# Optimization experiments

Measured on AMD Instinct MI355X. Metric: run time of the kernel, lower is better.

Reference implementation:

```python
import jax, jax.numpy as jnp
import numpy as np

SPAN = 128
STRIDE = 4
LQ = 2048
LKV = 512
H = 16
DQK = 64
DV = 64
DQ = 1024
DOUT = 1024
T = SPAN // STRIDE  # table depth (rows of the sparse QK table)


def _tables():
    # Static precomputation mirroring the torch __init__ meshgrid logic.
    row, col = np.meshgrid(np.arange(T), np.arange(LQ), indexing='ij')
    qi_col = np.ceil((col - (SPAN - 1)) / STRIDE).astype(np.int64) + row  # kv index per (r, j)
    qi_row = -STRIDE * qi_col + col
    valid = (qi_row >= 0) & (qi_row < SPAN) & (qi_col >= 0) & (qi_col < LKV)
    kidx = np.clip(qi_col, 0, LKV - 1)  # clipped gather index; invalid slots masked later
    return jnp.asarray(kidx), jnp.asarray(valid)

KIDX, VALID = _tables()  # both [T, LQ]


def setup_inputs() -> dict:
    key = jax.random.key(0)
    ks = jax.random.split(key, 7)
    s = 0.02
    return {
        'q': jax.random.normal(ks[0], (2, LQ, DQ), jnp.float32),
        'k': jax.random.normal(ks[1], (2, LKV, DQ), jnp.float32),
        'v': jax.random.normal(ks[2], (2, LKV, DQ), jnp.float32),
        'Wq': jax.random.normal(ks[3], (DQ, H * DQK), jnp.float32) * s,
        'Wk': jax.random.normal(ks[4], (DQ, H * DQK), jnp.float32) * s,
        'Wv': jax.random.normal(ks[5], (DQ, H * DV), jnp.float32) * s,
        'Wo': jax.random.normal(ks[6], (H * DV, DOUT), jnp.float32) * s,
    }


def reference(q, k, v, Wq, Wk, Wv, Wo):
    B = q.shape[0]
    Q = (q @ Wq).reshape(B, LQ, H, DQK).transpose(0, 2, 1, 3)    # [B,H,LQ,DQK]
    K = (k @ Wk).reshape(B, LKV, H, DQK).transpose(0, 2, 1, 3)   # [B,H,LKV,DQK]
    V = (v @ Wv).reshape(B, LKV, H, DV).transpose(0, 2, 1, 3)    # [B,H,LKV,DV]

    # Gather K/V by the strided-span index table: [B,H,T,LQ,d]
    Kg = K[:, :, KIDX, :]
    Vg = V[:, :, KIDX, :]

    scores = jnp.einsum('bhjd,bhtjd->bhtj', Q, Kg) / np.float32(np.sqrt(DQK))
    scores = jnp.where(VALID, scores, -jnp.inf)
    probs = jax.nn.softmax(scores, axis=2)          # softmax over table rows (dim 2 in torch)
    probs = jnp.where(VALID, probs, 0.0)

    O = jnp.einsum('bhtj,bhtjd->bhjd', probs, Vg)   # [B,H,LQ,DV]
    O = O.transpose(0, 2, 1, 3).reshape(B, LQ, H * DV)
    return O @ Wo
```

## Files before the change

### kernel.cpp

```cpp
#include <hip/hip_runtime.h>
#include <hip/hip_bf16.h>

typedef __bf16 bf16x8 __attribute__((ext_vector_type(8)));
typedef float  f32x4  __attribute__((ext_vector_type(4)));
typedef unsigned short u16;
typedef unsigned int   u32;

__device__ __forceinline__ u16 f2b(float x) {
  __bf16 b = (__bf16)x;
  return __builtin_bit_cast(u16, b);
}

__device__ __forceinline__ void gload_lds16(const u16* g, u16* l) {
  __builtin_amdgcn_global_load_lds(
      (const __attribute__((address_space(1))) void*)g,
      (__attribute__((address_space(3))) void*)l, 16, 0, 0);
}

__device__ __forceinline__ void cvt8_store(u16* dst, float4 a, float4 b) {
  union { u16 u[8]; uint4 v; } r;
  r.u[0] = f2b(a.x); r.u[1] = f2b(a.y); r.u[2] = f2b(a.z); r.u[3] = f2b(a.w);
  r.u[4] = f2b(b.x); r.u[5] = f2b(b.y); r.u[6] = f2b(b.z); r.u[7] = f2b(b.w);
  *(uint4*)dst = r.v;
}

__global__ __launch_bounds__(256) void prep_kernel(
    const float* __restrict__ W0, const float* __restrict__ W1,
    const float* __restrict__ W2, const float* __restrict__ W3,
    u16* __restrict__ T0, u16* __restrict__ T1, u16* __restrict__ T2, u16* __restrict__ T3)
{
  __shared__ float tile[32][33];
  int t = blockIdx.x;
  int z = t >> 10, rem = t & 1023;
  const float* W = (z == 0) ? W0 : (z == 1) ? W1 : (z == 2) ? W2 : W3;
  u16* T = (z == 0) ? T0 : (z == 1) ? T1 : (z == 2) ? T2 : T3;
  int tx = threadIdx.x & 31, ty = threadIdx.x >> 5;
  int c0 = (rem & 31) << 5, r0 = (rem >> 5) << 5;
#pragma unroll
  for (int i = 0; i < 4; ++i)
    tile[ty + i * 8][tx] = W[(size_t)(r0 + ty + i * 8) * 1024 + c0 + tx];
  __syncthreads();
#pragma unroll
  for (int i = 0; i < 4; ++i)
    T[(size_t)(c0 + ty + i * 8) * 1024 + r0 + tx] = f2b(tile[tx][ty + i * 8]);
}

__device__ __forceinline__ void compute_step(
    const u16* asc, const u16* bsc, int lane, int wm, int wn, f32x4 (&acc)[4][4])
{
#pragma unroll
  for (int kk = 0; kk < 2; ++kk) {
    bf16x8 af[4], bfr[4];
    int colb = (kk << 6) + ((lane >> 4) << 4);
#pragma unroll
    for (int m = 0; m < 4; ++m) {
      int r = (wm << 6) + (m << 4) + (lane & 15);
      af[m] = *(const bf16x8*)((const char*)asc + (r << 7) + (colb ^ ((r & 7) << 4)));
    }
#pragma unroll
    for (int n = 0; n < 4; ++n) {
      int r = (wn << 6) + (n << 4) + (lane & 15);
      bfr[n] = *(const bf16x8*)((const char*)bsc + (r << 7) + (colb ^ ((r & 7) << 4)));
    }
#pragma unroll
    for (int m = 0; m < 4; ++m)
#pragma unroll
      for (int n = 0; n < 4; ++n)
        acc[m][n] = __builtin_amdgcn_mfma_f32_16x16x32_bf16(af[m], bfr[n], acc[m][n], 0, 0, 0);
  }
}

__device__ __forceinline__ void stage_b(const u16* gB, u16* bs, int wave, int K, int k0) {
#pragma unroll
  for (int i = 0; i < 4; ++i) {
    int rb = (wave << 5) + (i << 3);
    gload_lds16(gB + (size_t)(i << 3) * K + k0, bs + (rb << 6));
  }
}

template <int OUTF32>
__device__ __forceinline__ void cwrite(
    void* C, int N, int row0, int col0, int lane, int wm, int wn, f32x4 (&acc)[4][4])
{
  const int crow = (lane >> 4) << 2;
  const int ccol = lane & 15;
#pragma unroll
  for (int m = 0; m < 4; ++m) {
#pragma unroll
    for (int n = 0; n < 4; ++n) {
      int r = row0 + (wm << 6) + (m << 4) + crow;
      int c = col0 + (wn << 6) + (n << 4) + ccol;
#pragma unroll
      for (int reg = 0; reg < 4; ++reg) {
        if (OUTF32) ((float*)C)[(size_t)(r + reg) * N + c] = acc[m][n][reg];
        else        ((u16*)C)[(size_t)(r + reg) * N + c] = f2b(acc[m][n][reg]);
      }
    }
  }
}

template <int OUTF32>
__device__ __forceinline__ void gemm_core(
    const u16* __restrict__ A, const u16* __restrict__ Bt, void* __restrict__ C,
    int N, int K, int row0, int col0,
    u16* As0, u16* As1, u16* Bs0, u16* Bs1)
{
  const int tid = threadIdx.x;
  const int wave = tid >> 6, lane = tid & 63;
  const int wm = wave >> 1, wn = wave & 1;
  f32x4 acc[4][4] = {};

  const int srow = lane >> 3, sslot = lane & 7;
  const int scol = ((sslot ^ srow) << 3);
  const u16* gA = A + (size_t)(row0 + (wave << 5) + srow) * K + scol;
  const u16* gB = Bt + (size_t)(col0 + (wave << 5) + srow) * K + scol;

  stage_b(gA, As0, wave, K, 0);
  stage_b(gB, Bs0, wave, K, 0);
  __syncthreads();

  u16 *asc = As0, *bsc = Bs0, *asn = As1, *bsn = Bs1;
  for (int k0 = 0; k0 < K; k0 += 64) {
    if (k0 + 64 < K) {
      stage_b(gA, asn, wave, K, k0 + 64);
      stage_b(gB, bsn, wave, K, k0 + 64);
    }
    compute_step(asc, bsc, lane, wm, wn, acc);
    __syncthreads();
    u16* t_;
    t_ = asc; asc = asn; asn = t_;
    t_ = bsc; bsc = bsn; bsn = t_;
  }
  cwrite<OUTF32>(C, N, row0, col0, lane, wm, wn, acc);
}

__device__ __forceinline__ void gemm_core_f32a(
    const float* __restrict__ Af,
    const u16* __restrict__ Bt, u16* __restrict__ C,
    int N, int K, int row0, int col0,
    u16* As0, u16* As1, u16* Bs0, u16* Bs1)
{
  const int tid = threadIdx.x;
  const int wave = tid >> 6, lane = tid & 63;
  const int wm = wave >> 1, wn = wave & 1;
  f32x4 acc[4][4] = {};

  const int srow = lane >> 3, sslot = lane & 7;
  const int scol = ((sslot ^ srow) << 3);
  const float* gAf = Af + (size_t)((wave << 5) + srow) * K + scol;
  const u16*  gB  = Bt + (size_t)(col0 + (wave << 5) + srow) * K + scol;
  const int awbase = (lane << 3);

  float4 a0[4], a1[4];
#pragma unroll
  for (int i = 0; i < 4; ++i) {
    const float* g = gAf + (size_t)(i << 3) * K;
    a0[i] = *(const float4*)g; a1[i] = *(const float4*)(g + 4);
  }
  stage_b(gB, Bs0, wave, K, 0);
#pragma unroll
  for (int i = 0; i < 4; ++i)
    cvt8_store(As0 + (((wave << 5) + (i << 3)) << 6) + awbase, a0[i], a1[i]);
  __syncthreads();

  u16 *asc = As0, *bsc = Bs0, *asn = As1, *bsn = Bs1;
  for (int k0 = 0; k0 < K; k0 += 64) {
    const bool more = (k0 + 64) < K;
    if (more) {
#pragma unroll
      for (int i = 0; i < 4; ++i) {
        const float* g = gAf + (size_t)(i << 3) * K + (k0 + 64);
        a0[i] = *(const float4*)g; a1[i] = *(const float4*)(g + 4);
      }
      stage_b(gB, bsn, wave, K, k0 + 64);
    }
    compute_step(asc, bsc, lane, wm, wn, acc);
    __syncthreads();
    if (more) {
#pragma unroll
      for (int i = 0; i < 4; ++i)
        cvt8_store(asn + (((wave << 5) + (i << 3)) << 6) + awbase, a0[i], a1[i]);
    }
    __syncthreads();
    u16* t_;
    t_ = asc; asc = asn; asn = t_;
    t_ = bsc; bsc = bsn; bsn = t_;
  }
  cwrite<0>(C, N, row0, col0, lane, wm, wn, acc);
}

template <int OUTF32>
__global__ __launch_bounds__(256, 2) void gemm_bt_kernel(
    const u16* __restrict__ A, const u16* __restrict__ Bt, void* __restrict__ C,
    int M, int N, int K)
{
  __shared__ u16 As[2][8192];
  __shared__ u16 Bs[2][8192];
  int bid = blockIdx.x;
  int t = (bid & 7) * 32 + (bid >> 3);
  const int bx = t & 7, by = t >> 3;
  gemm_core<OUTF32>(A, Bt, C, N, K, by << 7, bx << 7, As[0], As[1], Bs[0], Bs[1]);
}

__global__ __launch_bounds__(256, 2) void proj_kernel(
    const float* __restrict__ q, const float* __restrict__ k, const float* __restrict__ v,
    const u16* __restrict__ Wqt, const u16* __restrict__ Wkt, const u16* __restrict__ Wvt,
    u16* __restrict__ Qp, u16* __restrict__ KVp)
{
  __shared__ u16 As[2][8192];
  __shared__ u16 Bs[2][8192];
  int bid = blockIdx.x;
  int t = (bid & 7) * 48 + (bid >> 3);
  const float* Af; const u16* Bt; u16* C; int row0, col0;
  if (t < 256) {
    row0 = (t >> 3) << 7; col0 = (t & 7) << 7;
    Af = q + (size_t)row0 * 1024; Bt = Wqt; C = Qp;
  } else {
    int t2 = t - 256;
    row0 = (t2 >> 3) << 7; col0 = (t2 & 7) << 7;
    if (row0 < 1024) { Af = k + (size_t)row0 * 1024; Bt = Wkt; }
    else             { Af = v + (size_t)(row0 - 1024) * 1024; Bt = Wvt; }
    C = KVp;
  }
  gemm_core_f32a(Af, Bt, C, 1024, 1024, row0, col0, As[0], As[1], Bs[0], Bs[1]);
}

#define VTP 56
#define PLP 72
__global__ __launch_bounds__(256) void attn_kernel(
    const u16* __restrict__ Qp, const u16* __restrict__ Kp,
    const u16* __restrict__ Vp, u16* __restrict__ Ob)
{
  __shared__ u16 Ql[64 * 64];
  __shared__ u16 Kl[48 * 64];
  __shared__ u16 Vt[64 * VTP + 64];
  __shared__ u16 Pl[64 * PLP];

  const int jt = blockIdx.x, h = blockIdx.y, b = blockIdx.z;
  const int j0 = jt << 6;
  const int kbase = (j0 - 124) >> 2;
  const int tid = threadIdx.x;
  const int wave = tid >> 6, lane = tid & 63;

  const int srow = lane >> 3, sslot = lane & 7;
  const int scol = ((sslot ^ srow) << 3);
  for (int g = wave; g < 8; g += 4) {
    int r = (g << 3) + srow;
    const u16* ga = Qp + (((size_t)(b * 2048 + j0 + r)) << 10) + (h << 6) + scol;
    gload_lds16(ga, &Ql[g << 9]);
  }
  for (int g = wave; g < 6; g += 4) {
    int r = (g << 3) + srow;
    int key = kbase + r;
    key = key < 0 ? 0 : (key > 511 ? 511 : key);
    const u16* gk = Kp + (((size_t)(b * 512 + key)) << 10) + (h << 6) + scol;
    gload_lds16(gk, &Kl[g << 9]);
  }
  for (int idx = tid; idx < 48 * 8; idx += 256) {
    int row = idx >> 3, seg = idx & 7;
    int key = kbase + row;
    key = key < 0 ? 0 : (key > 511 ? 511 : key);
    uint4 x = *(const uint4*)(Vp + (((size_t)(b * 512 + key)) << 10) + (h << 6) + (seg << 3));
    int d0 = seg << 3;
    Vt[(d0 + 0) * VTP + row] = (u16)(x.x);
    Vt[(d0 + 1) * VTP + row] = (u16)(x.x >> 16);
    Vt[(d0 + 2) * VTP + row] = (u16)(x.y);
    Vt[(d0 + 3) * VTP + row] = (u16)(x.y >> 16);
    Vt[(d0 + 4) * VTP + row] = (u16)(x.z);
    Vt[(d0 + 5) * VTP + row] = (u16)(x.z >> 16);
    Vt[(d0 + 6) * VTP + row] = (u16)(x.w);
    Vt[(d0 + 7) * VTP + row] = (u16)(x.w >> 16);
  }
  if (tid < 64) *(uint4*)&Vt[tid * VTP + 48] = make_uint4(0, 0, 0, 0);
  else if (tid < 72) *(uint4*)&Vt[64 * VTP + ((tid - 64) << 3)] = make_uint4(0, 0, 0, 0);
  __syncthreads();

  f32x4 sacc[3] = {};
  const int frow_a = (wave << 4) + (lane & 15);
#pragma unroll
  for (int kk = 0; kk < 2; ++kk) {
    int colb = (kk << 6) + ((lane >> 4) << 4);
    bf16x8 aq = *(const bf16x8*)((const char*)Ql + (frow_a << 7) + (colb ^ ((frow_a & 7) << 4)));
#pragma unroll
    for (int nt = 0; nt < 3; ++nt) {
      int rk = (nt << 4) + (lane & 15);
      bf16x8 bk = *(const bf16x8*)((const char*)Kl + (rk << 7) + (colb ^ ((rk & 7) << 4)));
      sacc[nt] = __builtin_amdgcn_mfma_f32_16x16x32_bf16(aq, bk, sacc[nt], 0, 0, 0);
    }
  }

  const int rof = (wave << 2) + (lane >> 4);
  const int cb0 = lane & 15;
  bool vld[3]; float sc[3][4];
#pragma unroll
  for (int nt = 0; nt < 3; ++nt) {
    int c = cb0 + (nt << 4);
    vld[nt] = ((unsigned)(c - rof) < 32u) && (kbase + c >= 0);
#pragma unroll
    for (int r = 0; r < 4; ++r) sc[nt][r] = sacc[nt][r] * 0.125f;
  }
  float mx[4], rs[4];
#pragma unroll
  for (int r = 0; r < 4; ++r) {
    float m = -3.0e38f;
#pragma unroll
    for (int nt = 0; nt < 3; ++nt) m = vld[nt] ? fmaxf(m, sc[nt][r]) : m;
    m = fmaxf(m, __shfl_xor(m, 1));
    m = fmaxf(m, __shfl_xor(m, 2));
    m = fmaxf(m, __shfl_xor(m, 4));
    m = fmaxf(m, __shfl_xor(m, 8));
    mx[r] = m;
  }
#pragma unroll
  for (int r = 0; r < 4; ++r) {
    float s = 0.f;
#pragma unroll
    for (int nt = 0; nt < 3; ++nt) {
      float e = vld[nt] ? __expf(sc[nt][r] - mx[r]) : 0.f;
      sc[nt][r] = e;
      s += e;
    }
    s += __shfl_xor(s, 1);
    s += __shfl_xor(s, 2);
    s += __shfl_xor(s, 4);
    s += __shfl_xor(s, 8);
    rs[r] = 1.f / s;
  }
#pragma unroll
  for (int r = 0; r < 4; ++r) {
    int jq = (wave << 4) + ((lane >> 4) << 2) + r;
#pragma unroll
    for (int nt = 0; nt < 3; ++nt)
      Pl[jq * PLP + cb0 + (nt << 4)] = f2b(sc[nt][r] * rs[r]);
    Pl[jq * PLP + 48 + cb0] = 0;
  }
  __syncthreads();

  f32x4 oacc[4] = {};
#pragma unroll
  for (int kk = 0; kk < 2; ++kk) {
    int koff = (kk << 5) + ((lane >> 4) << 3);
    bf16x8 ap = *(const bf16x8*)&Pl[frow_a * PLP + koff];
#pragma unroll
    for (int nt = 0; nt < 4; ++nt) {
      int dr = (nt << 4) + (lane & 15);
      bf16x8 bv = *(const bf16x8*)&Vt[dr * VTP + koff];
      oacc[nt] = __builtin_amdgcn_mfma_f32_16x16x32_bf16(ap, bv, oacc[nt], 0, 0, 0);
    }
  }

#pragma unroll
  for (int nt = 0; nt < 4; ++nt) {
    int d = (nt << 4) + (lane & 15);
#pragma unroll
    for (int r = 0; r < 4; ++r) {
      int jq = (wave << 4) + ((lane >> 4) << 2) + r;
      Ob[(((size_t)(b * 2048 + j0 + jq)) << 10) + (h << 6) + d] = f2b(oacc[nt][r]);
    }
  }
}

extern "C" void kernel_launch(void* const* d_in, const int* in_sizes, int n_in,
                              void* d_out, int out_size, void* d_ws, size_t ws_size,
                              hipStream_t stream) {
  const float* q  = (const float*)d_in[0];
  const float* k  = (const float*)d_in[1];
  const float* v  = (const float*)d_in[2];
  const float* Wq = (const float*)d_in[3];
  const float* Wk = (const float*)d_in[4];
  const float* Wv = (const float*)d_in[5];
  const float* Wo = (const float*)d_in[6];

  char* ws = (char*)d_ws;
  const size_t MB = 1u << 20;
  u16* Wqt = (u16*)(ws + 0 * MB);
  u16* Wkt = (u16*)(ws + 2 * MB);
  u16* Wvt = (u16*)(ws + 4 * MB);
  u16* Wot = (u16*)(ws + 6 * MB);
  u16* Qp  = (u16*)(ws + 8 * MB);
  u16* Kp  = (u16*)(ws + 16 * MB);
  u16* Vp  = (u16*)(ws + 18 * MB);
  u16* Ob  = (u16*)(ws + 20 * MB);

  prep_kernel<<<4096, 256, 0, stream>>>(Wq, Wk, Wv, Wo, Wqt, Wkt, Wvt, Wot);
  proj_kernel<<<384, 256, 0, stream>>>(q, k, v, Wqt, Wkt, Wvt, Qp, Kp);
  attn_kernel<<<dim3(32, 16, 2), 256, 0, stream>>>(Qp, Kp, Vp, Ob);
  gemm_bt_kernel<1><<<256, 256, 0, stream>>>(Ob, Wot, d_out, 4096, 1024, 1024);
}
```

Before: 59.63 us.

## Move Wo transpose into attention kernel and remap attention block order

```diff
diff --git a/kernel.cpp b/kernel.cpp
--- a/kernel.cpp
+++ b/kernel.cpp
@@ -24,25 +24,31 @@
   *(uint4*)dst = r.v;
 }
 
+__device__ __forceinline__ void wtile_transpose(
+    const float* __restrict__ W, u16* __restrict__ T, int rem, float* tile )
+{
+  int tx = threadIdx.x & 31, ty = threadIdx.x >> 5;
+  int c0 = (rem & 31) << 5, r0 = (rem >> 5) << 5;
+#pragma unroll
+  for (int i = 0; i < 4; ++i)
+    tile[(ty + i * 8) * 33 + tx] = W[(size_t)(r0 + ty + i * 8) * 1024 + c0 + tx];
+  __syncthreads();
+#pragma unroll
+  for (int i = 0; i < 4; ++i)
+    T[(size_t)(c0 + ty + i * 8) * 1024 + r0 + tx] = f2b(tile[tx * 33 + ty + i * 8]);
+}
+
 __global__ __launch_bounds__(256) void prep_kernel(
     const float* __restrict__ W0, const float* __restrict__ W1,
-    const float* __restrict__ W2, const float* __restrict__ W3,
-    u16* __restrict__ T0, u16* __restrict__ T1, u16* __restrict__ T2, u16* __restrict__ T3)
-{
-  __shared__ float tile[32][33];
+    const float* __restrict__ W2,
+    u16* __restrict__ T0, u16* __restrict__ T1, u16* __restrict__ T2)
+{
+  __shared__ float tile[32 * 33];
   int t = blockIdx.x;
   int z = t >> 10, rem = t & 1023;
-  const float* W = (z == 0) ? W0 : (z == 1) ? W1 : (z == 2) ? W2 : W3;
-  u16* T = (z == 0) ? T0 : (z == 1) ? T1 : (z == 2) ? T2 : T3;
-  int tx = threadIdx.x & 31, ty = threadIdx.x >> 5;
-  int c0 = (rem & 31) << 5, r0 = (rem >> 5) << 5;
-#pragma unroll
-  for (int i = 0; i < 4; ++i)
-    tile[ty + i * 8][tx] = W[(size_t)(r0 + ty + i * 8) * 1024 + c0 + tx];
-  __syncthreads();
-#pragma unroll
-  for (int i = 0; i < 4; ++i)
-    T[(size_t)(c0 + ty + i * 8) * 1024 + r0 + tx] = f2b(tile[tx][ty + i * 8]);
+  const float* W = (z == 0) ? W0 : (z == 1) ? W1 : W2;
+  u16* T = (z == 0) ? T0 : (z == 1) ? T1 : T2;
+  wtile_transpose(W, T, rem, tile);
 }
 
 __device__ __forceinline__ void compute_step(
@@ -229,14 +235,21 @@
 #define PLP 72
 __global__ __launch_bounds__(256) void attn_kernel(
     const u16* __restrict__ Qp, const u16* __restrict__ Kp,
-    const u16* __restrict__ Vp, u16* __restrict__ Ob)
+    const u16* __restrict__ Vp, u16* __restrict__ Ob,
+    const float* __restrict__ W3, u16* __restrict__ T3)
 {
   __shared__ u16 Ql[64 * 64];
   __shared__ u16 Kl[48 * 64];
   __shared__ u16 Vt[64 * VTP + 64];
   __shared__ u16 Pl[64 * PLP];
 
-  const int jt = blockIdx.x, h = blockIdx.y, b = blockIdx.z;
+  const int bid = blockIdx.x;
+  if (bid >= 1024) {
+    wtile_transpose(W3, T3, bid - 1024, (float*)Ql);
+    return;
+  }
+  const int t = (bid & 7) * 128 + (bid >> 3);
+  const int jt = t & 31, h = (t >> 5) & 15, b = t >> 9;
   const int j0 = jt << 6;
   const int kbase = (j0 - 124) >> 2;
   const int tid = threadIdx.x;
@@ -382,8 +395,8 @@
   u16* Vp  = (u16*)(ws + 18 * MB);
   u16* Ob  = (u16*)(ws + 20 * MB);
 
-  prep_kernel<<<4096, 256, 0, stream>>>(Wq, Wk, Wv, Wo, Wqt, Wkt, Wvt, Wot);
+  prep_kernel<<<3072, 256, 0, stream>>>(Wq, Wk, Wv, Wqt, Wkt, Wvt);
   proj_kernel<<<384, 256, 0, stream>>>(q, k, v, Wqt, Wkt, Wvt, Qp, Kp);
-  attn_kernel<<<dim3(32, 16, 2), 256, 0, stream>>>(Qp, Kp, Vp, Ob);
+  attn_kernel<<<2048, 256, 0, stream>>>(Qp, Kp, Vp, Ob, Wo, Wot);
   gemm_bt_kernel<1><<<256, 256, 0, stream>>>(Ob, Wot, d_out, 4096, 1024, 1024);
 }
```

Result: faster. 58.24 us (-2.3%).
